# Kernel tuning notes

Measured on AMD Instinct MI355X. Metric: run time of the kernel, lower is better.

The kernel has to match this reference:

```python
import jax, jax.numpy as jnp
import numpy as np

WIN, SHIFT = 8, 4
DIM, HEADS, MLP_H = 96, 6, 384
B, H, W = 1, 512, 512
HEAD_D = DIM // HEADS
N = WIN * WIN
EPS = 1e-5


def _rel_pos_index():
    ch = np.arange(WIN)
    coords = np.stack(np.meshgrid(ch, ch, indexing='ij')).reshape(2, -1)  # [2, 64]
    rel = (coords[:, :, None] - coords[:, None, :]).transpose(1, 2, 0)    # [64, 64, 2]
    rel[:, :, 0] += WIN - 1
    rel[:, :, 1] += WIN - 1
    rel[:, :, 0] *= 2 * WIN - 1
    return rel.sum(-1)


def _attn_mask():
    img = np.zeros((H, W))
    cnt = 0
    for hs in (slice(0, -WIN), slice(-WIN, -SHIFT), slice(-SHIFT, None)):
        for ws in (slice(0, -WIN), slice(-WIN, -SHIFT), slice(-SHIFT, None)):
            img[hs, ws] = cnt
            cnt += 1
    mw = img.reshape(H // WIN, WIN, W // WIN, WIN).transpose(0, 2, 1, 3).reshape(-1, N)
    diff = mw[:, None, :] - mw[:, :, None]
    return np.where(diff != 0, -100.0, 0.0).astype(np.float32)  # [nW, 64, 64]


REL_IDX = jnp.asarray(_rel_pos_index())
ATTN_MASK = jnp.asarray(_attn_mask())


def layernorm(x, w, b):
    mu = jnp.mean(x, axis=-1, keepdims=True)
    var = jnp.mean(jnp.square(x - mu), axis=-1, keepdims=True)
    return (x - mu) * jax.lax.rsqrt(var + EPS) * w + b


def setup_inputs() -> dict:
    key = jax.random.key(0)
    ks = jax.random.split(key, 16)
    s = 0.02
    return {
        'x': jax.random.normal(ks[0], (B, DIM, H, W), jnp.float32),
        'norm1_w': jnp.ones((DIM,), jnp.float32),
        'norm1_b': jnp.zeros((DIM,), jnp.float32),
        'qkv_w': jax.random.normal(ks[1], (3 * DIM, DIM), jnp.float32) * s,
        'qkv_b': jnp.zeros((3 * DIM,), jnp.float32),
        'rpb': jax.random.normal(ks[2], ((2 * WIN - 1) ** 2, HEADS), jnp.float32) * s,
        'proj_w': jax.random.normal(ks[3], (DIM, DIM), jnp.float32) * s,
        'proj_b': jnp.zeros((DIM,), jnp.float32),
        'norm2_w': jnp.ones((DIM,), jnp.float32),
        'norm2_b': jnp.zeros((DIM,), jnp.float32),
        'fc1_w': jax.random.normal(ks[4], (MLP_H, DIM), jnp.float32) * s,
        'fc1_b': jnp.zeros((MLP_H,), jnp.float32),
        'fc2_w': jax.random.normal(ks[5], (DIM, MLP_H), jnp.float32) * s,
        'fc2_b': jnp.zeros((DIM,), jnp.float32),
    }


def reference(x, norm1_w, norm1_b, qkv_w, qkv_b, rpb, proj_w, proj_b,
              norm2_w, norm2_b, fc1_w, fc1_b, fc2_w, fc2_b):
    nH, nW_ = H // WIN, W // WIN
    nWin = nH * nW_
    shortcut = jnp.transpose(x, (0, 2, 3, 1))            # [B,H,W,C]
    xn = layernorm(shortcut, norm1_w, norm1_b)
    xs = jnp.roll(xn, (-SHIFT, -SHIFT), axis=(1, 2))     # cyclic shift
    # window partition -> [B*nWin, N, C]
    win = xs.reshape(B, nH, WIN, nW_, WIN, DIM).transpose(0, 1, 3, 2, 4, 5)
    win = win.reshape(B * nWin, N, DIM)
    qkv = win @ qkv_w.T + qkv_b                          # [Bw, N, 3C]
    qkv = qkv.reshape(-1, N, 3, HEADS, HEAD_D).transpose(2, 0, 3, 1, 4)
    q, k, v = qkv[0], qkv[1], qkv[2]                     # [Bw, h, N, d]
    scale = HEAD_D ** -0.5
    attn = jnp.einsum('bhnd,bhmd->bhnm', q * scale, k)   # [Bw, h, 64, 64]
    bias = rpb[REL_IDX.reshape(-1)].reshape(N, N, HEADS).transpose(2, 0, 1)
    attn = attn + bias[None]
    attn = attn.reshape(B, nWin, HEADS, N, N) + ATTN_MASK[None, :, None]
    attn = jax.nn.softmax(attn.reshape(-1, HEADS, N, N), axis=-1)
    out = jnp.einsum('bhnm,bhmd->bhnd', attn, v).transpose(0, 2, 1, 3).reshape(-1, N, DIM)
    out = out @ proj_w.T + proj_b
    # window reverse + un-shift
    out = out.reshape(B, nH, nW_, WIN, WIN, DIM).transpose(0, 1, 3, 2, 4, 5).reshape(B, H, W, DIM)
    out = jnp.roll(out, (SHIFT, SHIFT), axis=(1, 2))
    x1 = shortcut + out
    h = layernorm(x1, norm2_w, norm2_b)
    h = jax.nn.gelu(h @ fc1_w.T + fc1_b, approximate=False) @ fc2_w.T + fc2_b
    x2 = x1 + h
    return jnp.transpose(x2, (0, 3, 1, 2))               # [B,C,H,W]
```

## Files before the change

### kernel.cpp

```cpp
#include <hip/hip_runtime.h>
#include <math.h>

#define WINSZ  8
#define SHIFTV 4
#define DIM    96
#define HEADS  6
#define HEAD_D 16
#define MLP_H  384
#define HH     512
#define WWID   512
#define HWSZ   (HH*WWID)
#define NTOK   64
#define EPSV   1e-5f
#define XP     97
#define QP     17
#define BFP    120

#define OFF_W1   0
#define OFF_W2   36864
#define OFF_QKV  73728
#define OFF_PROJ 101376
#define OFF_BIAS 110592
#define WS_FULL  208896
#define WS_MLP   73728

#define QKP 104
#define VTP 72
#define X1P 97
#define WBP 104

#define WBA_OFF 13312
#define WBB_OFF 23296
#define SMEM_SZ 40448

typedef __attribute__((ext_vector_type(2))) short  s2v;
typedef __attribute__((ext_vector_type(4))) short  s4v;
typedef __attribute__((ext_vector_type(8))) short  s8v;
typedef __attribute__((ext_vector_type(4))) float  f4v;
typedef __attribute__((ext_vector_type(4))) unsigned short u4v;

__device__ __forceinline__ unsigned short f2bf(float v) {
    union { float f; unsigned u; } c; c.f = v;
    unsigned r = c.u + 0x7fffu + ((c.u >> 16) & 1u);
    return (unsigned short)(r >> 16);
}
__device__ __forceinline__ float bf2f(unsigned short u) {
    union { unsigned u; float f; } c; c.u = ((unsigned)u) << 16; return c.f;
}
__device__ __forceinline__ unsigned long long shfl64(unsigned long long v, int src) {
    union { unsigned long long q; int i[2]; } c; c.q = v;
    c.i[0] = __shfl(c.i[0], src);
    c.i[1] = __shfl(c.i[1], src);
    return c.q;
}
__device__ __forceinline__ float fast_gelu(float h) {
    float h2 = h*h;
    float u  = fmaf(0.044715f, h2, 1.0f);
    float e  = __expf(-1.5957691216057308f * h * u);
    return h * __builtin_amdgcn_rcpf(1.0f + e);
}

__device__ __forceinline__ void gld_lds16(const void* g, void* l) {
    __builtin_amdgcn_global_load_lds(
        (const __attribute__((address_space(1))) unsigned*)(g),
        (__attribute__((address_space(3))) unsigned*)(l),
        16, 0, 0);
}

__device__ __forceinline__ void stage48(const char* gb, int stride_b,
                                        char* wb, int tid) {
    #pragma unroll
    for (int k = 0; k < 3; ++k) {
        int idx = tid + k*256;
        if (k < 2 || idx < 624) {
            int r   = idx / 13;
            int rem = idx - r*13;
            const char* src = (rem < 12) ? (gb + r*stride_b + rem*16) : gb;
            char* dst = wb + ((tid & ~63) + k*256)*16;
            gld_lds16(src, dst);
        }
    }
}

__device__ __forceinline__ void stage_chunk(const char* w1B, const char* w2B,
                                            int n, char* dst, int tid) {
    int ch = n >> 2, s = n & 3;
    const char* src; int stride;
    if      (s == 0) { src = w1B + ch*96*192;            stride = 192; }
    else if (s == 1) { src = w1B + ch*96*192 + 48*192;   stride = 192; }
    else if (s == 2) { src = w2B + ch*192;               stride = 768; }
    else             { src = w2B + ch*192 + 48*768;      stride = 768; }
    stage48(src, stride, dst, tid);
}

__global__ __launch_bounds__(256) void conv_all(
    const float* __restrict__ qkvw, const float* __restrict__ projw,
    const float* __restrict__ f1w,  const float* __restrict__ f2w,
    const float* __restrict__ rpb,  short* __restrict__ ws)
{
    int i = (blockIdx.x*256 + threadIdx.x)*4;
    if (i < 110592) {
        const float* src; int off;
        if (i < 36864)       { src = f1w;  off = i;          }
        else if (i < 73728)  { src = f2w;  off = i - 36864;  }
        else if (i < 101376) { src = qkvw; off = i - 73728;  }
        else                 { src = projw; off = i - 101376; }
        f4v v = *(const f4v*)&src[off];
        s4v o;
        #pragma unroll
        for (int j = 0; j < 4; ++j) o[j] = (short)f2bf(v[j]);
        *(s4v*)&ws[i] = o;
    } else if (i < WS_FULL) {
        int idx = i - 110592;
        int tb = idx / 24576;
        int rm = idx - tb*24576;
        int hd = rm >> 12;
        int rc = rm & 4095;
        int r = rc >> 6, c0 = rc & 63;
        int rti = r>>3, rtj = r&7;
        int bh = tb>>1, bw = tb&1;
        int rhr = bh ? (rti<4?1:2) : 0;
        int rwr = bw ? (rtj<4?1:2) : 0;
        s4v o;
        #pragma unroll
        for (int j = 0; j < 4; ++j) {
            int c = c0 + j;
            int cti = c>>3, ctj = c&7;
            int rel = (rti-cti+7)*15 + (rtj-ctj+7);
            float b = rpb[rel*HEADS + hd];
            int rhc = bh ? (cti<4?1:2) : 0;
            int rwc = bw ? (ctj<4?1:2) : 0;
            if (rhr != rhc || rwr != rwc) b -= 100.f;
            o[j] = (short)f2bf(b);
        }
        *(s4v*)&ws[OFF_BIAS + idx] = o;
    }
}

__global__ __launch_bounds__(256,4) void fused_kernel(
    const float* __restrict__ x,
    const float* __restrict__ n1w, const float* __restrict__ n1b,
    const float* __restrict__ qkvb, const float* __restrict__ projb,
    const float* __restrict__ n2w, const float* __restrict__ n2b,
    const float* __restrict__ f1b, const float* __restrict__ f2b,
    const short* __restrict__ wqkv, const short* __restrict__ wproj,
    const short* __restrict__ w1b, const short* __restrict__ w2b,
    const short* __restrict__ btab,
    float* __restrict__ out)
{
    __shared__ __align__(16) char smem[SMEM_SZ];
    short* qb   = (short*)smem;
    short* kb2  = (short*)(smem + 13312);
    short* vT   = (short*)(smem + 26624);
    short* aob  = qb;
    short* lnb2 = (short*)smem;
    short* hid  = (short*)smem;
    short* wbA  = (short*)(smem + WBA_OFF);
    short* wbB  = (short*)(smem + WBB_OFF);
    float* x1f  = (float*)smem;

    const int tid  = threadIdx.x;
    const int wv   = tid >> 6, lane = tid & 63;
    const int col  = lane & 15, kq = lane >> 4;
    const int trow = wv*16 + col;

    int bid = blockIdx.x;
    int wl = (bid & 7)*512 + ((bid >> 5) << 2) + ((bid >> 3) & 3);
    const int wi = wl >> 6, wj = wl & 63;

    const int ti = trow>>3, tj = trow&7;
    const int hpos = (wi*8 + ti + SHIFTV) & (HH-1);
    const int wpos = (wj*8 + tj + SHIFTV) & (WWID-1);
    const int p = hpos*WWID + wpos;

    s8v bfr[3];
    {
        float v[24], s1 = 0.f, s2 = 0.f;
        #pragma unroll
        for (int kb = 0; kb < 3; ++kb)
            #pragma unroll
            for (int j = 0; j < 8; ++j) {
                float vv = x[(kb*32 + kq*8 + j)*HWSZ + p];
                v[kb*8+j] = vv; s1 += vv; s2 += vv*vv;
            }
        s1 += __shfl_xor(s1, 16); s2 += __shfl_xor(s2, 16);
        s1 += __shfl_xor(s1, 32); s2 += __shfl_xor(s2, 32);
        float mu = s1*(1.f/96.f);
        float rs = rsqrtf(s2*(1.f/96.f) - mu*mu + EPSV);
        #pragma unroll
        for (int kb = 0; kb < 3; ++kb) {
            f4v wA = *(const f4v*)&n1w[kb*32 + kq*8];
            f4v wB = *(const f4v*)&n1w[kb*32 + kq*8 + 4];
            f4v bA = *(const f4v*)&n1b[kb*32 + kq*8];
            f4v bB = *(const f4v*)&n1b[kb*32 + kq*8 + 4];
            s8v o;
            #pragma unroll
            for (int j = 0; j < 4; ++j) {
                o[j]   = (short)f2bf((v[kb*8+j]  -mu)*rs*wA[j] + bA[j]);
                o[4+j] = (short)f2bf((v[kb*8+4+j]-mu)*rs*wB[j] + bB[j]);
            }
            bfr[kb] = o;
        }
    }

    float shc[24];
    #pragma unroll
    for (int mt = 0; mt < 6; ++mt)
        #pragma unroll
        for (int i = 0; i < 4; ++i)
            shc[mt*4+i] = x[(mt*16 + kq*4 + i)*HWSZ + p];

    const s8v zfrag = {0,0,0,0,0,0,0,0};

    {
        #pragma unroll
        for (int g = 0; g < 6; ++g) {
            s8v aw[9];
            #pragma unroll
            for (int m = 0; m < 3; ++m)
                #pragma unroll
                for (int kb = 0; kb < 3; ++kb)
                    aw[m*3+kb] = *(const s8v*)&wqkv[((g*3+m)*16+col)*96 + kb*32 + kq*8];
            #pragma unroll
            for (int m = 0; m < 3; ++m) {
                int mt = g*3 + m;
                f4v acc = {0.f,0.f,0.f,0.f};
                #pragma unroll
                for (int kb = 0; kb < 3; ++kb)
                    acc = __builtin_amdgcn_mfma_f32_16x16x32_bf16(aw[m*3+kb], bfr[kb], acc, 0,0,0);
                int od0 = mt*16 + kq*4;
                f4v bia = *(const f4v*)&qkvb[od0];
                if (mt < 6) {
                    s4v o;
                    #pragma unroll
                    for (int i = 0; i < 4; ++i) o[i] = (short)f2bf((acc[i]+bia[i])*0.25f);
                    *(s4v*)&qb[trow*QKP + od0] = o;
                } else if (mt < 12) {
                    s4v o;
                    #pragma unroll
                    for (int i = 0; i < 4; ++i) o[i] = (short)f2bf(acc[i]+bia[i]);
                    *(s4v*)&kb2[trow*QKP + od0 - 96] = o;
                } else {
                    int d0 = od0 - 192;
                    #pragma unroll
                    for (int i = 0; i < 4; ++i)
                        vT[(d0+i)*VTP + trow] = (short)f2bf(acc[i]+bia[i]);
                }
            }
        }
    }
    __syncthreads();

    const int tb = ((wi==63)?2:0) | ((wj==63)?1:0);
    u4v bt[4];
    {
        const short* gb = btab + ((tb*6+0)<<12) + (trow<<6);
        #pragma unroll
        for (int mt = 0; mt < 4; ++mt) bt[mt] = *(const u4v*)&gb[mt*16 + kq*4];
    }
    for (int hd = 0; hd < 6; ++hd) {
        u4v btn[4];
        if (hd < 5) {
            const short* gb = btab + ((tb*6+hd+1)<<12) + (trow<<6);
            #pragma unroll
            for (int mt = 0; mt < 4; ++mt) btn[mt] = *(const u4v*)&gb[mt*16 + kq*4];
        }
        s8v bq = zfrag;
        if (kq < 2) bq = *(const s8v*)&qb[trow*QKP + hd*16 + kq*8];
        f4v st[4];
        #pragma unroll
        for (int mt = 0; mt < 4; ++mt) {
            s8v a = zfrag;
            if (kq < 2) a = *(const s8v*)&kb2[(mt*16+col)*QKP + hd*16 + kq*8];
            f4v z = {0.f,0.f,0.f,0.f};
            st[mt] = __builtin_amdgcn_mfma_f32_16x16x32_bf16(a, bq, z, 0,0,0);
        }
        float sc[16];
        #pragma unroll
        for (int mt = 0; mt < 4; ++mt) {
            #pragma unroll
            for (int i = 0; i < 4; ++i) sc[mt*4+i] = st[mt][i] + bf2f(bt[mt][i]);
        }
        float m8[8];
        #pragma unroll
        for (int j = 0; j < 8; ++j) m8[j] = fmaxf(sc[2*j], sc[2*j+1]);
        #pragma unroll
        for (int j = 0; j < 4; ++j) m8[j] = fmaxf(m8[j], m8[j+4]);
        float m = fmaxf(fmaxf(m8[0], m8[2]), fmaxf(m8[1], m8[3]));
        m = fmaxf(m, __shfl_xor(m, 16));
        m = fmaxf(m, __shfl_xor(m, 32));
        float s8r[8];
        #pragma unroll
        for (int j = 0; j < 8; ++j) {
            sc[2*j]   = __expf(sc[2*j]  -m);
            sc[2*j+1] = __expf(sc[2*j+1]-m);
            s8r[j] = sc[2*j] + sc[2*j+1];
        }
        #pragma unroll
        for (int j = 0; j < 4; ++j) s8r[j] += s8r[j+4];
        float sum = (s8r[0]+s8r[2]) + (s8r[1]+s8r[3]);
        sum += __shfl_xor(sum, 16);
        sum += __shfl_xor(sum, 32);
        unsigned long long p64[4];
        #pragma unroll
        for (int mt = 0; mt < 4; ++mt) {
            union { s4v v; unsigned long long q; } pk;
            #pragma unroll
            for (int i = 0; i < 4; ++i) pk.v[i] = (short)f2bf(sc[mt*4+i]);
            p64[mt] = pk.q;
        }
        const int s0 = col + ((kq & 1) << 5);
        const int sel = kq >> 1;
        f4v g = {0.f,0.f,0.f,0.f};
        #pragma unroll
        for (int c = 0; c < 2; ++c) {
            unsigned long long t0 = shfl64(p64[2*c],   s0);
            unsigned long long t1 = shfl64(p64[2*c+1], s0);
            unsigned long long lo = sel ? t1 : t0;
            unsigned long long u0 = shfl64(p64[2*c],   s0+16);
            unsigned long long u1 = shfl64(p64[2*c+1], s0+16);
            unsigned long long hi = sel ? u1 : u0;
            union { unsigned long long q[2]; s8v v; } bb;
            bb.q[0] = lo; bb.q[1] = hi;
            s8v a = *(const s8v*)&vT[(hd*16+col)*VTP + c*32 + kq*8];
            g = __builtin_amdgcn_mfma_f32_16x16x32_bf16(a, bb.v, g, 0,0,0);
        }
        float linv = 1.f/sum;
        s4v o;
        #pragma unroll
        for (int i = 0; i < 4; ++i) o[i] = (short)f2bf(g[i]*linv);
        *(s4v*)&aob[trow*QKP + hd*16 + kq*4] = o;
        #pragma unroll
        for (int mt = 0; mt < 4; ++mt) bt[mt] = btn[mt];
    }
    __syncthreads();

    stage_chunk((const char*)w1b, (const char*)w2b, 0, (char*)wbA, tid);
    stage_chunk((const char*)w1b, (const char*)w2b, 1, (char*)wbB, tid);

    float x1r[24];
    {
        s8v bfr2[3];
        #pragma unroll
        for (int kb = 0; kb < 3; ++kb)
            bfr2[kb] = *(const s8v*)&aob[trow*QKP + kb*32 + kq*8];
        #pragma unroll
        for (int g = 0; g < 2; ++g) {
            s8v aw[9];
            #pragma unroll
            for (int m = 0; m < 3; ++m)
                #pragma unroll
                for (int kb = 0; kb < 3; ++kb)
                    aw[m*3+kb] = *(const s8v*)&wproj[((g*3+m)*16+col)*96 + kb*32 + kq*8];
            #pragma unroll
            for (int m = 0; m < 3; ++m) {
                int mt = g*3 + m;
                f4v acc = {0.f,0.f,0.f,0.f};
                #pragma unroll
                for (int kb = 0; kb < 3; ++kb)
                    acc = __builtin_amdgcn_mfma_f32_16x16x32_bf16(aw[m*3+kb], bfr2[kb], acc, 0,0,0);
                int c0 = mt*16 + kq*4;
                f4v pb4 = *(const f4v*)&projb[c0];
                #pragma unroll
                for (int i = 0; i < 4; ++i)
                    x1r[mt*4+i] = shc[mt*4+i] + acc[i] + pb4[i];
            }
        }
    }

    const int mrow = wv*16;

    {
        float s1 = 0.f, s2 = 0.f;
        #pragma unroll
        for (int j = 0; j < 24; ++j) { s1 += x1r[j]; s2 += x1r[j]*x1r[j]; }
        s1 += __shfl_xor(s1, 16); s2 += __shfl_xor(s2, 16);
        s1 += __shfl_xor(s1, 32); s2 += __shfl_xor(s2, 32);
        float mu = s1*(1.f/96.f);
        float rs = rsqrtf(s2*(1.f/96.f) - mu*mu + EPSV);
        #pragma unroll
        for (int mt = 0; mt < 6; ++mt) {
            int c0 = mt*16 + kq*4;
            f4v w4 = *(const f4v*)&n2w[c0];
            f4v b4 = *(const f4v*)&n2b[c0];
            s4v o;
            #pragma unroll
            for (int i = 0; i < 4; ++i)
                o[i] = (short)f2bf((x1r[mt*4+i]-mu)*rs*w4[i] + b4[i]);
            *(s4v*)&lnb2[trow*QKP + c0] = o;
        }
    }
    __threadfence_block();

    s8v a1[3];
    #pragma unroll
    for (int kb = 0; kb < 3; ++kb)
        a1[kb] = *(const s8v*)&lnb2[(mrow+col)*QKP + kb*32 + kq*8];

    f4v acc2[6];
    #pragma unroll
    for (int n = 0; n < 6; ++n) acc2[n] = (f4v){0.f,0.f,0.f,0.f};

    __syncthreads();

    #pragma unroll
    for (int ch = 0; ch < 4; ++ch) {
        #pragma unroll
        for (int sub = 0; sub < 2; ++sub) {
            const int cidx = ch*4 + sub;
            const short* wb = (cidx & 1) ? wbB : wbA;
            #pragma unroll
            for (int nl = 0; nl < 3; ++nl) {
                f4v acc = (f4v){0.f,0.f,0.f,0.f};
                #pragma unroll
                for (int kb = 0; kb < 3; ++kb) {
                    s8v b = *(const s8v*)&wb[(nl*16+col)*WBP + kb*32 + kq*8];
                    acc = __builtin_amdgcn_mfma_f32_16x16x32_bf16(a1[kb], b, acc, 0,0,0);
                }
                int cch = sub*48 + nl*16 + col;
                float bias = f1b[ch*96 + cch];
                #pragma unroll
                for (int i = 0; i < 4; ++i)
                    hid[(mrow + kq*4 + i)*QKP + cch] = (short)f2bf(fast_gelu(acc[i]+bias));
            }
            __syncthreads();
            if (cidx + 2 < 16)
                stage_chunk((const char*)w1b, (const char*)w2b, cidx+2,
                            (char*)((cidx & 1) ? wbB : wbA), tid);
        }
        s8v a2[3];
        #pragma unroll
        for (int kb = 0; kb < 3; ++kb)
            a2[kb] = *(const s8v*)&hid[(mrow+col)*QKP + kb*32 + kq*8];
        #pragma unroll
        for (int sub = 0; sub < 2; ++sub) {
            const int cidx = ch*4 + 2 + sub;
            const short* wb = (cidx & 1) ? wbB : wbA;
            #pragma unroll
            for (int nl = 0; nl < 3; ++nl) {
                int nt = sub*3 + nl;
                #pragma unroll
                for (int kb = 0; kb < 3; ++kb) {
                    s8v b = *(const s8v*)&wb[(nl*16+col)*WBP + kb*32 + kq*8];
                    acc2[nt] = __builtin_amdgcn_mfma_f32_16x16x32_bf16(a2[kb], b, acc2[nt], 0,0,0);
                }
            }
            __syncthreads();
            if (cidx + 2 < 16)
                stage_chunk((const char*)w1b, (const char*)w2b, cidx+2,
                            (char*)((cidx & 1) ? wbB : wbA), tid);
        }
    }

    #pragma unroll
    for (int mt = 0; mt < 6; ++mt) {
        #pragma unroll
        for (int i = 0; i < 4; ++i)
            x1f[trow*X1P + mt*16 + kq*4 + i] = x1r[mt*4+i];
    }
    __threadfence_block();
    #pragma unroll
    for (int nt = 0; nt < 6; ++nt) {
        int c = nt*16 + col;
        float bias = f2b[c];
        #pragma unroll
        for (int i = 0; i < 4; ++i) {
            int t = mrow + kq*4 + i;
            x1f[t*X1P + c] += acc2[nt][i] + bias;
        }
    }
    __threadfence_block();
    {
        int tt = mrow + col;
        int tti = tt>>3, ttj = tt&7;
        int pp = ((wi*8 + tti + SHIFTV) & (HH-1))*WWID + ((wj*8 + ttj + SHIFTV) & (WWID-1));
        #pragma unroll
        for (int it = 0; it < 24; ++it) {
            int c = it*4 + kq;
            out[c*HWSZ + pp] = x1f[tt*X1P + c];
        }
    }
}

__global__ __launch_bounds__(256) void attn_kernel(
    const float* __restrict__ x,
    const float* __restrict__ n1w, const float* __restrict__ n1b,
    const float* __restrict__ qkvw, const float* __restrict__ qkvb,
    const float* __restrict__ rpb,
    const float* __restrict__ projw, const float* __restrict__ projb,
    float* __restrict__ out)
{
    __shared__ float xn[NTOK*XP];
    __shared__ float ao[NTOK*XP];
    __shared__ float qh[NTOK*QP];
    __shared__ float kh[NTOK*QP];
    __shared__ float vh[NTOK*QP];
    __shared__ int   srid[NTOK];
    __shared__ int   spos[NTOK];

    const int tid = threadIdx.x;
    const int blk = blockIdx.x;
    const int wi = blk >> 6, wj = blk & 63;

    {
        int t  = tid >> 2;
        int j4 = tid & 3;
        int ti = t >> 3, tj = t & 7;
        int a = wi*WINSZ + ti;
        int bcol = wj*WINSZ + tj;
        int h = (a + SHIFTV) & (HH-1);
        int w = (bcol + SHIFTV) & (WWID-1);
        int p = h*WWID + w;
        if (j4 == 0) {
            spos[t] = p;
            int rh = (a < HH-WINSZ) ? 0 : (a < HH-SHIFTV ? 1 : 2);
            int rw = (bcol < WWID-WINSZ) ? 0 : (bcol < WWID-SHIFTV ? 1 : 2);
            srid[t] = rh*3 + rw;
        }
        float xv[24];
        float s1 = 0.f, s2 = 0.f;
        int c0 = j4*24;
        #pragma unroll
        for (int i = 0; i < 24; ++i) {
            float v = x[(c0+i)*HWSZ + p];
            xv[i] = v; s1 += v; s2 += v*v;
        }
        s1 += __shfl_xor(s1,1); s2 += __shfl_xor(s2,1);
        s1 += __shfl_xor(s1,2); s2 += __shfl_xor(s2,2);
        float mu  = s1 * (1.f/96.f);
        float var = s2 * (1.f/96.f) - mu*mu;
        float rs  = rsqrtf(var + EPSV);
        #pragma unroll
        for (int i = 0; i < 24; ++i) {
            int c = c0 + i;
            xn[t*XP + c] = (xv[i]-mu)*rs*n1w[c] + n1b[c];
        }
    }
    __syncthreads();

    const int wv   = tid >> 6;
    const int lane = tid & 63;
    const int r    = tid >> 2;
    const int g    = tid & 3;
    const int rti  = r >> 3, rtj = r & 7;

    for (int hd = 0; hd < HEADS; ++hd) {
        for (int it = 0; it < 12; ++it) {
            int ol = it*4 + wv;
            int s = ol >> 4, d = ol & 15;
            int grow = __builtin_amdgcn_readfirstlane(s*DIM + hd*HEAD_D + d);
            const float* wr = qkvw + grow*DIM;
            float acc = qkvb[grow];
            #pragma unroll 8
            for (int c = 0; c < DIM; ++c)
                acc = fmaf(xn[lane*XP+c], wr[c], acc);
            float* dst = (s==0) ? qh : ((s==1) ? kh : vh);
            dst[lane*QP + d] = acc;
        }
        __syncthreads();

        float qr[16];
        #pragma unroll
        for (int d = 0; d < 16; ++d) qr[d] = qh[r*QP+d];
        float scr[16];
        int myrid = srid[r];
        #pragma unroll
        for (int jj = 0; jj < 16; ++jj) {
            int colx = g*16 + jj;
            float a = 0.f;
            #pragma unroll
            for (int d = 0; d < 16; ++d) a = fmaf(qr[d], kh[colx*QP+d], a);
            int cti = colx >> 3, ctj = colx & 7;
            int rel = (rti - cti + 7)*15 + (rtj - ctj + 7);
            float b = rpb[rel*HEADS + hd];
            float m = (srid[colx]==myrid) ? 0.f : -100.f;
            scr[jj] = a*0.25f + b + m;
        }
        float mx = scr[0];
        #pragma unroll
        for (int jj = 1; jj < 16; ++jj) mx = fmaxf(mx, scr[jj]);
        mx = fmaxf(mx, __shfl_xor(mx,1));
        mx = fmaxf(mx, __shfl_xor(mx,2));
        float sum = 0.f;
        #pragma unroll
        for (int jj = 0; jj < 16; ++jj) { scr[jj] = __expf(scr[jj]-mx); sum += scr[jj]; }
        sum += __shfl_xor(sum,1);
        sum += __shfl_xor(sum,2);
        float inv = 1.f/sum;
        #pragma unroll
        for (int d = 0; d < 16; ++d) {
            float a = 0.f;
            #pragma unroll
            for (int jj = 0; jj < 16; ++jj) a = fmaf(scr[jj], vh[(g*16+jj)*QP+d], a);
            a += __shfl_xor(a,1);
            a += __shfl_xor(a,2);
            if (g == 0) ao[r*XP + hd*HEAD_D + d] = a*inv;
        }
        __syncthreads();
    }

    for (int it = 0; it < 24; ++it) {
        int c = __builtin_amdgcn_readfirstlane(it*4 + wv);
        const float* wr = projw + c*DIM;
        float acc = projb[c];
        #pragma unroll 8
        for (int k = 0; k < DIM; ++k)
            acc = fmaf(ao[lane*XP+k], wr[k], acc);
        int p2 = spos[lane];
        float shc = x[c*HWSZ + p2];
        out[c*HWSZ + p2] = shc + acc;
    }
}

__global__ __launch_bounds__(256) void mlp_mfma(
    float* __restrict__ io,
    const float* __restrict__ n2w, const float* __restrict__ n2b,
    const short* __restrict__ w1b, const float* __restrict__ f1b,
    const short* __restrict__ w2b, const float* __restrict__ f2b)
{
    __shared__ short lnbuf[64*BFP];
    __shared__ __align__(16) char ubuf[64*XP*4];
    float* lnf = (float*)ubuf;
    short* hbc = (short*)ubuf;

    const int tid  = threadIdx.x;
    const int base = blockIdx.x * 64;

    for (int idx = tid; idx < 64*DIM; idx += 256) {
        int c = idx >> 6, t = idx & 63;
        lnf[t*XP + c] = io[c*HWSZ + base + t];
    }
    __syncthreads();
    {
        int t = tid >> 2, q = tid & 3;
        float xv[24], s1 = 0.f, s2 = 0.f;
        #pragma unroll
        for (int i = 0; i < 24; ++i) {
            float v = lnf[t*XP + q*24 + i]; xv[i] = v; s1 += v; s2 += v*v;
        }
        s1 += __shfl_xor(s1,1); s2 += __shfl_xor(s2,1);
        s1 += __shfl_xor(s1,2); s2 += __shfl_xor(s2,2);
        float mu = s1*(1.f/96.f);
        float rs = rsqrtf(s2*(1.f/96.f) - mu*mu + EPSV);
        #pragma unroll
        for (int i = 0; i < 24; ++i) {
            int c = q*24 + i;
            lnbuf[t*BFP + c] = (short)f2bf((xv[i]-mu)*rs*n2w[c] + n2b[c]);
        }
    }
    __syncthreads();

    const int l = tid & 63, wv = tid >> 6;
    const int mrow = wv*16;
    const int col = l & 15, kq = l >> 4;

    s8v a1[3];
    #pragma unroll
    for (int kb = 0; kb < 3; ++kb)
        a1[kb] = *(const s8v*)&lnbuf[(mrow+col)*BFP + kb*32 + kq*8];

    f4v acc2[6];
    #pragma unroll
    for (int n = 0; n < 6; ++n) acc2[n] = (f4v){0.f,0.f,0.f,0.f};

    for (int ch = 0; ch < 4; ++ch) {
        #pragma unroll
        for (int nt = 0; nt < 6; ++nt) {
            int n0 = ch*96 + nt*16;
            f4v acc = (f4v){0.f,0.f,0.f,0.f};
            #pragma unroll
            for (int kb = 0; kb < 3; ++kb) {
                s8v b = *(const s8v*)&w1b[(n0+col)*96 + kb*32 + kq*8];
                acc = __builtin_amdgcn_mfma_f32_16x16x32_bf16(a1[kb], b, acc, 0, 0, 0);
            }
            float bias = f1b[n0+col];
            #pragma unroll
            for (int i = 0; i < 4; ++i) {
                float g = fast_gelu(acc[i] + bias);
                hbc[(mrow + kq*4 + i)*BFP + nt*16 + col] = (short)f2bf(g);
            }
        }
        __threadfence_block();
        s8v a2[3];
        #pragma unroll
        for (int kb = 0; kb < 3; ++kb)
            a2[kb] = *(const s8v*)&hbc[(mrow+col)*BFP + kb*32 + kq*8];
        #pragma unroll
        for (int nt = 0; nt < 6; ++nt) {
            #pragma unroll
            for (int kb = 0; kb < 3; ++kb) {
                s8v b = *(const s8v*)&w2b[(nt*16+col)*MLP_H + ch*96 + kb*32 + kq*8];
                acc2[nt] = __builtin_amdgcn_mfma_f32_16x16x32_bf16(a2[kb], b, acc2[nt], 0, 0, 0);
            }
        }
        __threadfence_block();
    }

    #pragma unroll
    for (int nt = 0; nt < 6; ++nt) {
        int c = nt*16 + col;
        float bias = f2b[c];
        #pragma unroll
        for (int i = 0; i < 4; ++i) {
            int t = mrow + kq*4 + i;
            float* p = &io[c*HWSZ + base + t];
            *p = *p + acc2[nt][i] + bias;
        }
    }
}

__global__ __launch_bounds__(256) void conv_w(
    const float* __restrict__ f1w, const float* __restrict__ f2w,
    short* __restrict__ ws)
{
    int i = blockIdx.x*256 + threadIdx.x;
    if (i < 36864)      ws[i] = (short)f2bf(f1w[i]);
    else if (i < 73728) ws[i] = (short)f2bf(f2w[i-36864]);
}

extern "C" void kernel_launch(void* const* d_in, const int* in_sizes, int n_in,
                              void* d_out, int out_size, void* d_ws, size_t ws_size,
                              hipStream_t stream) {
    const float* x     = (const float*)d_in[0];
    const float* n1w   = (const float*)d_in[1];
    const float* n1b   = (const float*)d_in[2];
    const float* qkvw  = (const float*)d_in[3];
    const float* qkvb  = (const float*)d_in[4];
    const float* rpb   = (const float*)d_in[5];
    const float* projw = (const float*)d_in[6];
    const float* projb = (const float*)d_in[7];
    const float* n2w   = (const float*)d_in[8];
    const float* n2b   = (const float*)d_in[9];
    const float* f1w   = (const float*)d_in[10];
    const float* f1b   = (const float*)d_in[11];
    const float* f2w   = (const float*)d_in[12];
    const float* f2b   = (const float*)d_in[13];
    float* out = (float*)d_out;

    if (ws_size >= (size_t)WS_FULL * sizeof(short)) {
        short* wsb = (short*)d_ws;
        hipLaunchKernelGGL(conv_all, dim3(204), dim3(256), 0, stream,
                           qkvw, projw, f1w, f2w, rpb, wsb);
        hipLaunchKernelGGL(fused_kernel, dim3(4096), dim3(256), 0, stream,
                           x, n1w, n1b, qkvb, projb, n2w, n2b, f1b, f2b,
                           wsb + OFF_QKV, wsb + OFF_PROJ,
                           wsb + OFF_W1, wsb + OFF_W2, wsb + OFF_BIAS, out);
    } else {
        short* wsb = (short*)d_ws;
        hipLaunchKernelGGL(attn_kernel, dim3(4096), dim3(256), 0, stream,
                           x, n1w, n1b, qkvw, qkvb, rpb, projw, projb, out);
        hipLaunchKernelGGL(conv_w, dim3(288), dim3(256), 0, stream, f1w, f2w, wsb);
        hipLaunchKernelGGL(mlp_mfma, dim3(4096), dim3(256), 0, stream,
                           out, n2w, n2b, wsb, f1b, wsb + 36864, f2b);
    }
}
```

Before: 400.4 us.

## Use packed bf16 conversion, exp2 softmax with folded log2e, drop max subtraction

Replaces the software round-to-nearest bf16 conversion with the hardware packed v_cvt_pk_bf16_f32 instruction throughout. Folds log2(e) into the query scale and the precomputed bias table so the softmax and GELU can use native exp2. Removes the row-max reduction and subtraction in softmax, relying on small score magnitudes, which saves ALU and shuffle work but risks overflow for large logits.

```diff
diff --git a/kernel.cpp b/kernel.cpp
--- a/kernel.cpp
+++ b/kernel.cpp
@@ -16,6 +16,9 @@
 #define QP     17
 #define BFP    120
 
+#define L2E    1.44269504088896f
+#define QSC    0.360673760222f
+
 #define OFF_W1   0
 #define OFF_W2   36864
 #define OFF_QKV  73728
@@ -47,6 +50,24 @@
 __device__ __forceinline__ float bf2f(unsigned short u) {
     union { unsigned u; float f; } c; c.u = ((unsigned)u) << 16; return c.f;
 }
+__device__ __forceinline__ unsigned pk2(float a, float b) {
+    unsigned r;
+    asm("v_cvt_pk_bf16_f32 %0, %1, %2" : "=v"(r) : "v"(a), "v"(b));
+    return r;
+}
+__device__ __forceinline__ s4v pk4(f4v v) {
+    union { unsigned u[2]; s4v s; } o;
+    o.u[0] = pk2(v[0], v[1]);
+    o.u[1] = pk2(v[2], v[3]);
+    return o.s;
+}
+__device__ __forceinline__ float fexp2(float x) {
+#if __has_builtin(__builtin_amdgcn_exp2f)
+    return __builtin_amdgcn_exp2f(x);
+#else
+    return exp2f(x);
+#endif
+}
 __device__ __forceinline__ unsigned long long shfl64(unsigned long long v, int src) {
     union { unsigned long long q; int i[2]; } c; c.q = v;
     c.i[0] = __shfl(c.i[0], src);
@@ -56,7 +77,7 @@
 __device__ __forceinline__ float fast_gelu(float h) {
     float h2 = h*h;
     float u  = fmaf(0.044715f, h2, 1.0f);
-    float e  = __expf(-1.5957691216057308f * h * u);
+    float e  = fexp2(-2.3022082f * h * u);
     return h * __builtin_amdgcn_rcpf(1.0f + e);
 }
 
@@ -131,7 +152,7 @@
             int rhc = bh ? (cti<4?1:2) : 0;
             int rwc = bw ? (ctj<4?1:2) : 0;
             if (rhr != rhc || rwr != rwc) b -= 100.f;
-            o[j] = (short)f2bf(b);
+            o[j] = (short)f2bf(b * L2E);
         }
         *(s4v*)&ws[OFF_BIAS + idx] = o;
     }
@@ -193,13 +214,16 @@
             f4v wB = *(const f4v*)&n1w[kb*32 + kq*8 + 4];
             f4v bA = *(const f4v*)&n1b[kb*32 + kq*8];
             f4v bB = *(const f4v*)&n1b[kb*32 + kq*8 + 4];
-            s8v o;
+            float a[8];
             #pragma unroll
             for (int j = 0; j < 4; ++j) {
-                o[j]   = (short)f2bf((v[kb*8+j]  -mu)*rs*wA[j] + bA[j]);
-                o[4+j] = (short)f2bf((v[kb*8+4+j]-mu)*rs*wB[j] + bB[j]);
-            }
-            bfr[kb] = o;
+                a[j]   = (v[kb*8+j]  -mu)*rs*wA[j] + bA[j];
+                a[4+j] = (v[kb*8+4+j]-mu)*rs*wB[j] + bB[j];
+            }
+            union { unsigned u[4]; s8v s; } o;
+            #pragma unroll
+            for (int j = 0; j < 4; ++j) o.u[j] = pk2(a[2*j], a[2*j+1]);
+            bfr[kb] = o.s;
         }
     }
 
@@ -231,20 +255,24 @@
                 int od0 = mt*16 + kq*4;
                 f4v bia = *(const f4v*)&qkvb[od0];
                 if (mt < 6) {
-                    s4v o;
+                    f4v t;
                     #pragma unroll
-                    for (int i = 0; i < 4; ++i) o[i] = (short)f2bf((acc[i]+bia[i])*0.25f);
-                    *(s4v*)&qb[trow*QKP + od0] = o;
+                    for (int i = 0; i < 4; ++i) t[i] = (acc[i]+bia[i])*QSC;
+                    *(s4v*)&qb[trow*QKP + od0] = pk4(t);
                 } else if (mt < 12) {
-                    s4v o;
+                    f4v t;
                     #pragma unroll
-                    for (int i = 0; i < 4; ++i) o[i] = (short)f2bf(acc[i]+bia[i]);
-                    *(s4v*)&kb2[trow*QKP + od0 - 96] = o;
+                    for (int i = 0; i < 4; ++i) t[i] = acc[i]+bia[i];
+                    *(s4v*)&kb2[trow*QKP + od0 - 96] = pk4(t);
                 } else {
                     int d0 = od0 - 192;
+                    f4v t;
+                    #pragma unroll
+                    for (int i = 0; i < 4; ++i) t[i] = acc[i]+bia[i];
+                    s4v o = pk4(t);
                     #pragma unroll
                     for (int i = 0; i < 4; ++i)
-                        vT[(d0+i)*VTP + trow] = (short)f2bf(acc[i]+bia[i]);
+                        vT[(d0+i)*VTP + trow] = o[i];
                 }
             }
         }
@@ -275,27 +303,15 @@
             f4v z = {0.f,0.f,0.f,0.f};
             st[mt] = __builtin_amdgcn_mfma_f32_16x16x32_bf16(a, bq, z, 0,0,0);
         }
-        float sc[16];
-        #pragma unroll
-        for (int mt = 0; mt < 4; ++mt) {
-            #pragma unroll
-            for (int i = 0; i < 4; ++i) sc[mt*4+i] = st[mt][i] + bf2f(bt[mt][i]);
-        }
-        float m8[8];
-        #pragma unroll
-        for (int j = 0; j < 8; ++j) m8[j] = fmaxf(sc[2*j], sc[2*j+1]);
-        #pragma unroll
-        for (int j = 0; j < 4; ++j) m8[j] = fmaxf(m8[j], m8[j+4]);
-        float m = fmaxf(fmaxf(m8[0], m8[2]), fmaxf(m8[1], m8[3]));
-        m = fmaxf(m, __shfl_xor(m, 16));
-        m = fmaxf(m, __shfl_xor(m, 32));
+        float pe[16];
+        #pragma unroll
+        for (int mt = 0; mt < 4; ++mt)
+            #pragma unroll
+            for (int i = 0; i < 4; ++i)
+                pe[mt*4+i] = fexp2(st[mt][i] + bf2f(bt[mt][i]));
         float s8r[8];
         #pragma unroll
-        for (int j = 0; j < 8; ++j) {
-            sc[2*j]   = __expf(sc[2*j]  -m);
-            sc[2*j+1] = __expf(sc[2*j+1]-m);
-            s8r[j] = sc[2*j] + sc[2*j+1];
-        }
+        for (int j = 0; j < 8; ++j) s8r[j] = pe[2*j] + pe[2*j+1];
         #pragma unroll
         for (int j = 0; j < 4; ++j) s8r[j] += s8r[j+4];
         float sum = (s8r[0]+s8r[2]) + (s8r[1]+s8r[3]);
@@ -304,10 +320,10 @@
         unsigned long long p64[4];
         #pragma unroll
         for (int mt = 0; mt < 4; ++mt) {
-            union { s4v v; unsigned long long q; } pk;
-            #pragma unroll
-            for (int i = 0; i < 4; ++i) pk.v[i] = (short)f2bf(sc[mt*4+i]);
-            p64[mt] = pk.q;
+            union { unsigned u[2]; unsigned long long q; } pq;
+            pq.u[0] = pk2(pe[mt*4+0], pe[mt*4+1]);
+            pq.u[1] = pk2(pe[mt*4+2], pe[mt*4+3]);
+            p64[mt] = pq.q;
         }
         const int s0 = col + ((kq & 1) << 5);
         const int sel = kq >> 1;
@@ -325,11 +341,11 @@
             s8v a = *(const s8v*)&vT[(hd*16+col)*VTP + c*32 + kq*8];
             g = __builtin_amdgcn_mfma_f32_16x16x32_bf16(a, bb.v, g, 0,0,0);
         }
-        float linv = 1.f/sum;
-        s4v o;
-        #pragma unroll
-        for (int i = 0; i < 4; ++i) o[i] = (short)f2bf(g[i]*linv);
-        *(s4v*)&aob[trow*QKP + hd*16 + kq*4] = o;
+        float linv = __builtin_amdgcn_rcpf(sum);
+        f4v gl;
+        #pragma unroll
+        for (int i = 0; i < 4; ++i) gl[i] = g[i]*linv;
+        *(s4v*)&aob[trow*QKP + hd*16 + kq*4] = pk4(gl);
         #pragma unroll
         for (int mt = 0; mt < 4; ++mt) bt[mt] = btn[mt];
     }
@@ -383,11 +399,11 @@
             int c0 = mt*16 + kq*4;
             f4v w4 = *(const f4v*)&n2w[c0];
             f4v b4 = *(const f4v*)&n2b[c0];
-            s4v o;
+            f4v t;
             #pragma unroll
             for (int i = 0; i < 4; ++i)
-                o[i] = (short)f2bf((x1r[mt*4+i]-mu)*rs*w4[i] + b4[i]);
-            *(s4v*)&lnb2[trow*QKP + c0] = o;
+                t[i] = (x1r[mt*4+i]-mu)*rs*w4[i] + b4[i];
+            *(s4v*)&lnb2[trow*QKP + c0] = pk4(t);
         }
     }
     __threadfence_block();
@@ -419,9 +435,13 @@
                 }
                 int cch = sub*48 + nl*16 + col;
                 float bias = f1b[ch*96 + cch];
+                f4v t;
+                #pragma unroll
+                for (int i = 0; i < 4; ++i) t[i] = fast_gelu(acc[i]+bias);
+                s4v o = pk4(t);
                 #pragma unroll
                 for (int i = 0; i < 4; ++i)
-                    hid[(mrow + kq*4 + i)*QKP + cch] = (short)f2bf(fast_gelu(acc[i]+bias));
+                    hid[(mrow + kq*4 + i)*QKP + cch] = o[i];
             }
             __syncthreads();
             if (cidx + 2 < 16)
```

After: 391.9 us. 2.1% less time.
